# Optimization experiments

Measured on AMD Instinct MI355X. Metric: run time of the kernel, lower is better.

The kernel has to match this reference:

```python
import jax, jax.numpy as jnp
import numpy as np

D_MODEL = 1024
D_STATE = 64
D_CONV = 4
EXPAND = 2
HEADDIM = 64
FFN_MULT = 3
MEM_DIM = 256
D_INNER = EXPAND * D_MODEL            # 2048
NHEADS = D_INNER // HEADDIM           # 32
CONV_DIM = D_INNER + 2 * D_STATE      # x, B, C channels through the causal conv
D_IN_PROJ = 2 * D_INNER + 2 * D_STATE + NHEADS  # z, xBC, dt
FFN_HID = FFN_MULT * D_MODEL


def _rms(x, eps=1e-6):
    return x * jax.lax.rsqrt(jnp.mean(x * x, axis=-1, keepdims=True) + eps)


def _mamba2(u, in_proj_w, conv_w, conv_b, dt_bias, A_log, D_param, mnorm_w, out_proj_w):
    # u: [B, L, d_model]
    Bsz, L, _ = u.shape
    zxbcdt = u @ in_proj_w.T                                  # [B, L, D_IN_PROJ]
    z = zxbcdt[..., :D_INNER]                                 # gate branch
    xBC = zxbcdt[..., D_INNER:D_INNER + CONV_DIM]
    dt = zxbcdt[..., D_INNER + CONV_DIM:]                     # [B, L, H]
    # causal depthwise conv1d (kernel D_CONV) + silu
    xp = jnp.pad(xBC, ((0, 0), (D_CONV - 1, 0), (0, 0)))
    xBC = sum(xp[:, k:k + L, :] * conv_w[:, k] for k in range(D_CONV)) + conv_b
    xBC = jax.nn.silu(xBC)
    xh = xBC[..., :D_INNER].reshape(Bsz, L, NHEADS, HEADDIM)  # [B, L, H, P]
    Bm = xBC[..., D_INNER:D_INNER + D_STATE]                  # [B, L, N] (ngroups=1)
    Cm = xBC[..., D_INNER + D_STATE:]                         # [B, L, N]
    dt = jax.nn.softplus(dt + dt_bias)                        # [B, L, H]
    dA = jnp.exp(dt * (-jnp.exp(A_log)))                      # [B, L, H]

    def step(h, inp):
        # h: [B, H, P, N]
        da, dtt, xt, bt, ct = inp
        h = da[:, :, None, None] * h + jnp.einsum('bh,bhp,bn->bhpn', dtt, xt, bt)
        y = jnp.einsum('bhpn,bn->bhp', h, ct)
        return h, y

    h0 = jnp.zeros((Bsz, NHEADS, HEADDIM, D_STATE), u.dtype)
    xs = (jnp.moveaxis(dA, 1, 0), jnp.moveaxis(dt, 1, 0), jnp.moveaxis(xh, 1, 0),
          jnp.moveaxis(Bm, 1, 0), jnp.moveaxis(Cm, 1, 0))
    _, ys = jax.lax.scan(step, h0, xs)                        # ys: [L, B, H, P]
    y = jnp.moveaxis(ys, 0, 1) + D_param[None, None, :, None] * xh
    y = y.reshape(Bsz, L, D_INNER)
    y = _rms(y * jax.nn.silu(z)) * mnorm_w                    # RMSNormGated
    return y @ out_proj_w.T


def setup_inputs() -> dict:
    key = jax.random.key(0)
    ks = jax.random.split(key, 12)
    B, L = 1, 2048
    s = 0.02
    return {
        'x': jax.random.normal(ks[0], (B, L, D_MODEL), jnp.float32),
        'x0': jax.random.normal(ks[1], (B, L, D_MODEL), jnp.float32),
        'mem': jax.random.normal(ks[2], (B, MEM_DIM), jnp.float32),
        'resid_mix': jnp.stack([jnp.ones(D_MODEL), jnp.zeros(D_MODEL)]),
        'ssm_scale': jnp.ones(D_MODEL),
        'mlp_scale': jnp.ones(D_MODEL),
        'ssm_norm_w': jnp.ones(D_MODEL),
        'ffn_norm_w': jnp.ones(D_MODEL),
        'in_proj_w': jax.random.normal(ks[3], (D_IN_PROJ, D_MODEL), jnp.float32) * s,
        'conv_w': jax.random.normal(ks[4], (CONV_DIM, D_CONV), jnp.float32) * 0.2,
        'conv_b': jnp.zeros(CONV_DIM),
        'dt_bias': jax.random.uniform(ks[5], (NHEADS,), jnp.float32, -2.0, 0.0),
        'A_log': jnp.log(jnp.linspace(1.0, 16.0, NHEADS).astype(jnp.float32)),
        'D_param': jnp.ones(NHEADS),
        'mnorm_w': jnp.ones(D_INNER),
        'out_proj_w': jax.random.normal(ks[6], (D_MODEL, D_INNER), jnp.float32) * s,
        'gate_up_w': jax.random.normal(ks[7], (2 * FFN_HID, D_MODEL), jnp.float32) * s,
        'down_w': jax.random.normal(ks[8], (D_MODEL, FFN_HID), jnp.float32) * s,
    }


def reference(x, x0, mem, resid_mix, ssm_scale, mlp_scale, ssm_norm_w, ffn_norm_w,
              in_proj_w, conv_w, conv_b, dt_bias, A_log, D_param, mnorm_w,
              out_proj_w, gate_up_w, down_w):
    # residual mixing (USE_MEMORY=0, so mem path is inert)
    x = resid_mix[0][None, None, :] * x + resid_mix[1][None, None, :] * x0
    y = _mamba2(_rms(x) * ssm_norm_w, in_proj_w, conv_w, conv_b, dt_bias,
                A_log, D_param, mnorm_w, out_proj_w)
    x = x + ssm_scale[None, None, :] * y
    # SwiGLU FFN
    h = _rms(x) * ffn_norm_w
    gu = h @ gate_up_w.T
    gate, up = jnp.split(gu, 2, axis=-1)
    x = x + mlp_scale[None, None, :] * ((jax.nn.silu(gate) * up) @ down_w.T)
    return x
```

## Files before the change

### kernel.cpp

```cpp
#include <hip/hip_runtime.h>
#include <hip/hip_bf16.h>
#include <math.h>

#define LSEQ 2048
#define DMODEL 1024
#define DINNER 2048
#define NHEADS 32
#define HEADDIM 64
#define DSTATE 64
#define CONVDIM 2176
#define XBCDT_W 2304
#define FFNHID 3072

typedef float f32x4 __attribute__((ext_vector_type(4)));
typedef __bf16 bf16x8 __attribute__((ext_vector_type(8)));
typedef __hip_bfloat16 bf16;

__device__ __forceinline__ float siluf(float x){ return x / (1.0f + expf(-x)); }

#define GLOAD_LDS16(gp, lp) __builtin_amdgcn_global_load_lds( \
    (const __attribute__((address_space(1))) void*)(gp), \
    (__attribute__((address_space(3))) void*)(lp), 16, 0, 0)

__device__ __forceinline__ float block_reduce_sum_256(float v){
  #pragma unroll
  for (int o = 32; o > 0; o >>= 1) v += __shfl_down(v, o, 64);
  __shared__ float sh[4];
  int lane = threadIdx.x & 63;
  int w = threadIdx.x >> 6;
  if (lane == 0) sh[w] = v;
  __syncthreads();
  return sh[0] + sh[1] + sh[2] + sh[3];
}

__device__ __forceinline__ ushort bf16bits(float f){
  __hip_bfloat16 h = __float2bfloat16(f);
  return *reinterpret_cast<ushort*>(&h);
}
__device__ __forceinline__ float bfu(ushort u){
  union { float f; unsigned int i; } w; w.i = ((unsigned int)u) << 16; return w.f;
}

__device__ __forceinline__ int swz64(int r, int c){
  return r*64 + ((((c>>3) ^ (r&7)))<<3) + (c&7);
}

__global__ __launch_bounds__(256) void k_castmix(
    const float* __restrict__ w0, const float* __restrict__ w1,
    const float* __restrict__ w2, const float* __restrict__ w3,
    bf16* __restrict__ d0, bf16* __restrict__ d1,
    bf16* __restrict__ d2, bf16* __restrict__ d3,
    const float* __restrict__ x, const float* __restrict__ x0,
    const float* __restrict__ rm, const float* __restrict__ nw,
    float* __restrict__ xres, bf16* __restrict__ u)
{
  int tid = threadIdx.x;
  if (blockIdx.x < 15616){
    int idx = blockIdx.x * 256 + tid;
    const float* s; bf16* d; int valid;
    if (idx < 1114112)      { s = w0; d = d0; valid = 1089536; }
    else if (idx < 1638400) { idx -= 1114112; s = w1; d = d1; valid = 524288; }
    else if (idx < 3211264) { idx -= 1638400; s = w2; d = d2; valid = 1572864; }
    else                    { idx -= 3211264; s = w3; d = d3; valid = 786432; }
    float4 v = (idx < valid) ? *(const float4*)(s + (size_t)idx * 4)
                             : make_float4(0.f, 0.f, 0.f, 0.f);
    ushort4 r;
    r.x = bf16bits(v.x); r.y = bf16bits(v.y); r.z = bf16bits(v.z); r.w = bf16bits(v.w);
    *(ushort4*)(d + (size_t)idx * 4) = r;
    return;
  }
  int row = blockIdx.x - 15616;
  float4 xv  = ((const float4*)(x  + (size_t)row * DMODEL))[tid];
  float4 x0v = ((const float4*)(x0 + (size_t)row * DMODEL))[tid];
  float4 r0 = ((const float4*)rm)[tid];
  float4 r1 = ((const float4*)(rm + DMODEL))[tid];
  float4 a;
  a.x = r0.x*xv.x + r1.x*x0v.x; a.y = r0.y*xv.y + r1.y*x0v.y;
  a.z = r0.z*xv.z + r1.z*x0v.z; a.w = r0.w*xv.w + r1.w*x0v.w;
  ((float4*)(xres + (size_t)row * DMODEL))[tid] = a;
  float ss = a.x*a.x + a.y*a.y + a.z*a.z + a.w*a.w;
  ss = block_reduce_sum_256(ss);
  float inv = rsqrtf(ss / (float)DMODEL + 1e-6f);
  float4 nv = ((const float4*)nw)[tid];
  ushort4 o;
  o.x = bf16bits(a.x*inv*nv.x); o.y = bf16bits(a.y*inv*nv.y);
  o.z = bf16bits(a.z*inv*nv.z); o.w = bf16bits(a.w*inv*nv.w);
  *(ushort4*)(u + (size_t)row * DMODEL + tid*4) = o;
}

__device__ __forceinline__ void xcdswz2(int &bx, int &by){
  int gx = gridDim.x;
  int nblk = gx * gridDim.y;
  int flat = by * gx + bx;
  flat = (flat & 7) * (nblk >> 3) + (flat >> 3);
  by = flat / gx; bx = flat - by * gx;
}

__device__ __forceinline__ void gemm_mainloop128(
    const bf16* __restrict__ A, const bf16* __restrict__ W,
    int ld, int Klen, bf16* As, bf16* Ws, f32x4 acc[4][4])
{
  int tid = threadIdx.x, lane = tid & 63, wid = tid >> 6;
  int wm = (wid >> 1) * 64, wn = (wid & 1) * 64;
  int r16 = lane & 15, g8 = lane >> 4;
  int srow = lane >> 2;
  int scol = ((lane & 3) ^ (srow & 3) ^ ((srow >> 2) & 3)) * 8;
  const bf16* ga0 = A + (size_t)(wid*32 + srow) * ld + scol;
  const bf16* ga1 = ga0 + (size_t)16 * ld;
  const bf16* gw0 = W + (size_t)(wid*32 + srow) * ld + scol;
  const bf16* gw1 = gw0 + (size_t)16 * ld;
  GLOAD_LDS16(ga0, As + wid*1024);
  GLOAD_LDS16(ga1, As + wid*1024 + 512);
  GLOAD_LDS16(gw0, Ws + wid*1024);
  GLOAD_LDS16(gw1, Ws + wid*1024 + 512);
  __syncthreads();
  int cur = 0;
  int s4 = ((r16 & 3) ^ ((r16 >> 2) & 3)) * 8;
  for (int k0 = 0; k0 < Klen; k0 += 32){
    if (k0 + 32 < Klen){
      int nb = (cur ^ 1) * 4096;
      GLOAD_LDS16(ga0 + k0 + 32, As + nb + wid*1024);
      GLOAD_LDS16(ga1 + k0 + 32, As + nb + wid*1024 + 512);
      GLOAD_LDS16(gw0 + k0 + 32, Ws + nb + wid*1024);
      GLOAD_LDS16(gw1 + k0 + 32, Ws + nb + wid*1024 + 512);
    }
    int cb = cur * 4096;
    bf16x8 af[4], bfr[4];
    #pragma unroll
    for (int i = 0; i < 4; ++i)
      af[i] = *(const bf16x8*)(As + cb + (wm + i*16 + r16)*32 + (g8*8 ^ s4));
    #pragma unroll
    for (int j = 0; j < 4; ++j)
      bfr[j] = *(const bf16x8*)(Ws + cb + (wn + j*16 + r16)*32 + (g8*8 ^ s4));
    #pragma unroll
    for (int i = 0; i < 4; ++i)
      #pragma unroll
      for (int j = 0; j < 4; ++j)
        acc[i][j] = __builtin_amdgcn_mfma_f32_16x16x32_bf16(af[i], bfr[j], acc[i][j], 0, 0, 0);
    __syncthreads();
    cur ^= 1;
  }
}

__global__ __launch_bounds__(256) void k_gemm_inproj(
    const bf16* __restrict__ A, const bf16* __restrict__ Wfull,
    bf16* __restrict__ zbuf, bf16* __restrict__ xbcdt)
{
  __shared__ __align__(16) bf16 As[2*4096];
  __shared__ __align__(16) bf16 Ws[2*4096];
  int bx = blockIdx.x, by = blockIdx.y;
  xcdswz2(bx, by);
  f32x4 acc[4][4];
  #pragma unroll
  for (int i = 0; i < 4; ++i)
    #pragma unroll
    for (int j = 0; j < 4; ++j) acc[i][j] = (f32x4){0.f,0.f,0.f,0.f};
  gemm_mainloop128(A + (size_t)(by*128)*DMODEL, Wfull + (size_t)(bx*128)*DMODEL,
                   DMODEL, DMODEL, As, Ws, acc);
  int tid = threadIdx.x, lane = tid & 63, wid = tid >> 6;
  int wm = (wid >> 1) * 64, wn = (wid & 1) * 64;
  int r16 = lane & 15, g8 = lane >> 4;
  bf16* Cp; int ldc, col0;
  if (bx < 16){ Cp = zbuf;  ldc = DINNER;  col0 = bx*128; }
  else        { Cp = xbcdt; ldc = XBCDT_W; col0 = (bx-16)*128; }
  #pragma unroll
  for (int i = 0; i < 4; ++i){
    int row = by*128 + wm + i*16 + g8*4;
    #pragma unroll
    for (int j = 0; j < 4; ++j){
      int col = col0 + wn + j*16 + r16;
      #pragma unroll
      for (int r = 0; r < 4; ++r)
        Cp[(size_t)(row + r) * ldc + col] = __float2bfloat16(acc[i][j][r]);
    }
  }
}

__global__ __launch_bounds__(256) void k_gemm_splitk(
    const bf16* __restrict__ A, const bf16* __restrict__ W,
    float* __restrict__ P, int Kfull, int Kq, int N)
{
  __shared__ __align__(16) bf16 As[2*4096];
  __shared__ __align__(16) bf16 Ws[2*4096];
  int gx = gridDim.x, gxy = gx * gridDim.y;
  int nblk = gxy * gridDim.z;
  int flat = blockIdx.z * gxy + blockIdx.y * gx + blockIdx.x;
  flat = (flat & 7) * (nblk >> 3) + (flat >> 3);
  int z = flat / gxy; int rem = flat - z * gxy;
  int by = rem / gx, bx = rem - by * gx;
  f32x4 acc[4][4];
  #pragma unroll
  for (int i = 0; i < 4; ++i)
    #pragma unroll
    for (int j = 0; j < 4; ++j) acc[i][j] = (f32x4){0.f,0.f,0.f,0.f};
  gemm_mainloop128(A + (size_t)(by*128)*Kfull + z*Kq,
                   W + (size_t)(bx*128)*Kfull + z*Kq,
                   Kfull, Kq, As, Ws, acc);
  float* Pz = P + (size_t)z * LSEQ * N;
  int tid = threadIdx.x, lane = tid & 63, wid = tid >> 6;
  int wm = (wid >> 1) * 64, wn = (wid & 1) * 64;
  int r16 = lane & 15, g8 = lane >> 4;
  #pragma unroll
  for (int i = 0; i < 4; ++i){
    int row = by*128 + wm + i*16 + g8*4;
    #pragma unroll
    for (int j = 0; j < 4; ++j){
      int col = bx*128 + wn + j*16 + r16;
      #pragma unroll
      for (int r = 0; r < 4; ++r)
        Pz[(size_t)(row + r) * N + col] = acc[i][j][r];
    }
  }
}

__global__ __launch_bounds__(256) void k_gemm_ffn(
    const bf16* __restrict__ A, const bf16* __restrict__ Wg, const bf16* __restrict__ Wu,
    bf16* __restrict__ act, int K)
{
  __shared__ __align__(16) bf16 As[2*4096];
  __shared__ __align__(16) bf16 Ws[2*4096];
  int bx = blockIdx.x, by = blockIdx.y;
  xcdswz2(bx, by);
  int tid = threadIdx.x, lane = tid & 63, wid = tid >> 6;
  int wm = (wid >> 1) * 64, wc = (wid & 1) * 32;
  int r16 = lane & 15, g8 = lane >> 4;
  int srow = lane >> 2;
  int scol = ((lane & 3) ^ (srow & 3) ^ ((srow >> 2) & 3)) * 8;
  const bf16* ga0 = A + (size_t)(by*128 + wid*32 + srow) * K + scol;
  const bf16* ga1 = ga0 + (size_t)16 * K;
  const bf16* gwsrc = (wid < 2) ? Wg : Wu;
  const bf16* gw0 = gwsrc + (size_t)(bx*64 + (wid & 1)*32 + srow) * K + scol;
  const bf16* gw1 = gw0 + (size_t)16 * K;
  f32x4 accg[4][2], accu[4][2];
  #pragma unroll
  for (int i = 0; i < 4; ++i)
    #pragma unroll
    for (int j = 0; j < 2; ++j){
      accg[i][j] = (f32x4){0.f,0.f,0.f,0.f};
      accu[i][j] = (f32x4){0.f,0.f,0.f,0.f};
    }
  GLOAD_LDS16(ga0, As + wid*1024);
  GLOAD_LDS16(ga1, As + wid*1024 + 512);
  GLOAD_LDS16(gw0, Ws + wid*1024);
  GLOAD_LDS16(gw1, Ws + wid*1024 + 512);
  __syncthreads();
  int cur = 0;
  int s4 = ((r16 & 3) ^ ((r16 >> 2) & 3)) * 8;
  for (int k0 = 0; k0 < K; k0 += 32){
    if (k0 + 32 < K){
      int nb = (cur ^ 1) * 4096;
      GLOAD_LDS16(ga0 + k0 + 32, As + nb + wid*1024);
      GLOAD_LDS16(ga1 + k0 + 32, As + nb + wid*1024 + 512);
      GLOAD_LDS16(gw0 + k0 + 32, Ws + nb + wid*1024);
      GLOAD_LDS16(gw1 + k0 + 32, Ws + nb + wid*1024 + 512);
    }
    int cb = cur * 4096;
    bf16x8 af[4], gf[2], uf[2];
    #pragma unroll
    for (int i = 0; i < 4; ++i)
      af[i] = *(const bf16x8*)(As + cb + (wm + i*16 + r16)*32 + (g8*8 ^ s4));
    #pragma unroll
    for (int j = 0; j < 2; ++j){
      int gr = wc + j*16 + r16;
      int ur = 64 + wc + j*16 + r16;
      gf[j] = *(const bf16x8*)(Ws + cb + gr*32 + (g8*8 ^ s4));
      uf[j] = *(const bf16x8*)(Ws + cb + ur*32 + (g8*8 ^ s4));
    }
    #pragma unroll
    for (int i = 0; i < 4; ++i)
      #pragma unroll
      for (int j = 0; j < 2; ++j){
        accg[i][j] = __builtin_amdgcn_mfma_f32_16x16x32_bf16(af[i], gf[j], accg[i][j], 0, 0, 0);
        accu[i][j] = __builtin_amdgcn_mfma_f32_16x16x32_bf16(af[i], uf[j], accu[i][j], 0, 0, 0);
      }
    __syncthreads();
    cur ^= 1;
  }
  #pragma unroll
  for (int i = 0; i < 4; ++i){
    int row = by*128 + wm + i*16 + g8*4;
    #pragma unroll
    for (int j = 0; j < 2; ++j){
      int col = bx*64 + wc + j*16 + r16;
      #pragma unroll
      for (int r = 0; r < 4; ++r){
        float g = accg[i][j][r], u = accu[i][j][r];
        act[(size_t)(row + r) * FFNHID + col] = __float2bfloat16(siluf(g) * u);
      }
    }
  }
}

__global__ __launch_bounds__(256) void k_convdt(
    const bf16* __restrict__ xbcdt, const float* __restrict__ cw,
    const float* __restrict__ cb, const float* __restrict__ dtb,
    const float* __restrict__ alog, bf16* __restrict__ xbc,
    float* __restrict__ dtv, float* __restrict__ lav)
{
  int idx = blockIdx.x * 256 + threadIdx.x;
  int l = idx / 552, q = idx - l * 552;
  if (l >= LSEQ) return;
  if (q < 544){
    int c = q * 4;
    float4 bv = *(const float4*)(cb + c);
    float acc0 = bv.x, acc1 = bv.y, acc2 = bv.z, acc3 = bv.w;
    float4 w0 = *(const float4*)(cw + (size_t)(c+0)*4);
    float4 w1 = *(const float4*)(cw + (size_t)(c+1)*4);
    float4 w2 = *(const float4*)(cw + (size_t)(c+2)*4);
    float4 w3 = *(const float4*)(cw + (size_t)(c+3)*4);
    const float* w0p = (const float*)&w0;
    const float* w1p = (const float*)&w1;
    const float* w2p = (const float*)&w2;
    const float* w3p = (const float*)&w3;
    #pragma unroll
    for (int k = 0; k < 4; ++k){
      int t = l + k - 3;
      if (t < 0) continue;
      ushort4 rv = *(const ushort4*)(xbcdt + (size_t)t * XBCDT_W + c);
      acc0 = fmaf(bfu(rv.x), w0p[k], acc0);
      acc1 = fmaf(bfu(rv.y), w1p[k], acc1);
      acc2 = fmaf(bfu(rv.z), w2p[k], acc2);
      acc3 = fmaf(bfu(rv.w), w3p[k], acc3);
    }
    ushort4 o;
    o.x = bf16bits(siluf(acc0)); o.y = bf16bits(siluf(acc1));
    o.z = bf16bits(siluf(acc2)); o.w = bf16bits(siluf(acc3));
    *(ushort4*)(xbc + (size_t)l * CONVDIM + c) = o;
  } else {
    int h0 = (q - 544) * 4;
    ushort4 rv = *(const ushort4*)(xbcdt + (size_t)l * XBCDT_W + CONVDIM + h0);
    float raws[4] = { bfu(rv.x), bfu(rv.y), bfu(rv.z), bfu(rv.w) };
    #pragma unroll
    for (int i = 0; i < 4; ++i){
      float raw = raws[i] + dtb[h0 + i];
      float d = (raw > 20.f) ? raw : log1pf(expf(raw));
      dtv[l * NHEADS + h0 + i] = d;
      lav[l * NHEADS + h0 + i] = -expf(alog[h0 + i]) * d;
    }
  }
}

__global__ __launch_bounds__(256) void k_scanA(
    const bf16* __restrict__ xbc, const float* __restrict__ dtv,
    const float* __restrict__ lav, float* __restrict__ T, float* __restrict__ ctot)
{
  __shared__ __bf16 sXw[4096];
  __shared__ __bf16 sBt[4096];
  __shared__ float scum[64], swt[64];
  int h = blockIdx.x >> 5, c = blockIdx.x & 31;
  int tid = threadIdx.x, t0 = c * 64;
  if (tid < 64){
    float cum = lav[(size_t)(t0 + tid) * NHEADS + h];
    #pragma unroll
    for (int o = 1; o < 64; o <<= 1){
      float v = __shfl_up(cum, o, 64);
      if (tid >= o) cum += v;
    }
    scum[tid] = cum;
  }
  __syncthreads();
  float Lc = scum[63];
  if (tid < 64)
    swt[tid] = expf(Lc - scum[tid]) * dtv[(size_t)(t0 + tid) * NHEADS + h];
  __syncthreads();
  for (int idx = tid; idx < 512; idx += 256){
    int j = idx >> 3, n0 = (idx & 7) * 8;
    const bf16* rb = xbc + (size_t)(t0 + j) * CONVDIM;
    bf16x8 x8 = *(const bf16x8*)(rb + h * HEADDIM + n0);
    bf16x8 b8 = *(const bf16x8*)(rb + DINNER + n0);
    float wj = swt[j];
    #pragma unroll
    for (int e = 0; e < 8; ++e){
      sXw[swz64(n0 + e, j)] = (__bf16)((float)x8[e] * wj);
      sBt[swz64(n0 + e, j)] = b8[e];
    }
  }
  __syncthreads();
  int lane = tid & 63, wid = tid >> 6;
  int wr = (wid >> 1) * 32, wc = (wid & 1) * 32;
  int r16 = lane & 15, g8 = lane >> 4;
  f32x4 acc[2][2];
  #pragma unroll
  for (int i = 0; i < 2; ++i)
    #pragma unroll
    for (int j = 0; j < 2; ++j) acc[i][j] = (f32x4){0.f,0.f,0.f,0.f};
  #pragma unroll
  for (int kk = 0; kk < 2; ++kk){
    int ks = kk*4 + g8;
    bf16x8 a[2], b[2];
    #pragma unroll
    for (int i = 0; i < 2; ++i){
      int row = wr + i*16 + r16;
      a[i] = *(const bf16x8*)(sXw + row*64 + ((ks ^ (row&7))<<3));
    }
    #pragma unroll
    for (int j = 0; j < 2; ++j){
      int row = wc + j*16 + r16;
      b[j] = *(const bf16x8*)(sBt + row*64 + ((ks ^ (row&7))<<3));
    }
    #pragma unroll
    for (int i = 0; i < 2; ++i)
      #pragma unroll
      for (int j = 0; j < 2; ++j)
        acc[i][j] = __builtin_amdgcn_mfma_f32_16x16x32_bf16(a[i], b[j], acc[i][j], 0, 0, 0);
  }
  float* Tb = T + (size_t)blockIdx.x * 4096;
  #pragma unroll
  for (int i = 0; i < 2; ++i)
    #pragma unroll
    for (int j = 0; j < 2; ++j)
      #pragma unroll
      for (int r = 0; r < 4; ++r){
        int p = wr + i*16 + g8*4 + r, n = wc + j*16 + r16;
        Tb[p*64 + n] = acc[i][j][r];
      }
  if (tid == 0) ctot[blockIdx.x] = expf(Lc);
}

__global__ __launch_bounds__(256) void k_scanB(float* __restrict__ T, const float* __restrict__ ctot)
{
  int h = blockIdx.x >> 3, e = blockIdx.x & 7;
  int tid = threadIdx.x;
  size_t off = (size_t)e * 512 + tid * 2;
  float s0 = 0.f, s1 = 0.f;
  for (int c0 = 0; c0 < 32; c0 += 8){
    float2 tv[8]; float cts[8];
    #pragma unroll
    for (int q = 0; q < 8; ++q){
      cts[q] = ctot[h * 32 + c0 + q];
      tv[q] = *(const float2*)&T[(size_t)(h * 32 + c0 + q) * 4096 + off];
    }
    #pragma unroll
    for (int q = 0; q < 8; ++q){
      size_t base = (size_t)(h * 32 + c0 + q) * 4096 + off;
      *(float2*)&T[base] = make_float2(s0, s1);
      s0 = fmaf(cts[q], s0, tv[q].x);
      s1 = fmaf(cts[q], s1, tv[q].y);
    }
  }
}

__global__ __launch_bounds__(256) void k_scanC(
    const bf16* __restrict__ xbc, const float* __restrict__ Sin,
    const float* __restrict__ dtv, const float* __restrict__ lav,
    const float* __restrict__ Dp, bf16* __restrict__ y)
{
  __shared__ __bf16 sC[4096];
  __shared__ __bf16 sBS[4096];
  __shared__ __bf16 sXt[4096];
  __shared__ __bf16 sXr[4096];
  __shared__ __bf16 sSb[4096];
  __shared__ float scum[64], sdt[64];
  int h = blockIdx.x >> 5, c = blockIdx.x & 31;
  int tid = threadIdx.x, t0 = c * 64;
  if (tid < 64){
    float cum = lav[(size_t)(t0 + tid) * NHEADS + h];
    #pragma unroll
    for (int o = 1; o < 64; o <<= 1){
      float v = __shfl_up(cum, o, 64);
      if (tid >= o) cum += v;
    }
    scum[tid] = cum;
    sdt[tid] = dtv[(size_t)(t0 + tid) * NHEADS + h];
  }
  for (int idx = tid; idx < 512; idx += 256){
    int j = idx >> 3, n0 = (idx & 7) * 8;
    const bf16* rb = xbc + (size_t)(t0 + j) * CONVDIM;
    bf16x8 x8 = *(const bf16x8*)(rb + h * HEADDIM + n0);
    bf16x8 c8 = *(const bf16x8*)(rb + DINNER + DSTATE + n0);
    bf16x8 b8 = *(const bf16x8*)(rb + DINNER + n0);
    *(bf16x8*)(sC  + swz64(j, n0)) = c8;
    *(bf16x8*)(sBS + swz64(j, n0)) = b8;
    *(bf16x8*)(sXr + swz64(j, n0)) = x8;
    const float* sp = Sin + (size_t)blockIdx.x * 4096 + j*64 + n0;
    float4 s0 = *(const float4*)sp;
    float4 s1 = *(const float4*)(sp + 4);
    bf16x8 sv;
    sv[0] = (__bf16)s0.x; sv[1] = (__bf16)s0.y; sv[2] = (__bf16)s0.z; sv[3] = (__bf16)s0.w;
    sv[4] = (__bf16)s1.x; sv[5] = (__bf16)s1.y; sv[6] = (__bf16)s1.z; sv[7] = (__bf16)s1.w;
    *(bf16x8*)(sSb + swz64(j, n0)) = sv;
    #pragma unroll
    for (int e = 0; e < 8; ++e)
      sXt[swz64(n0 + e, j)] = x8[e];
  }
  __syncthreads();
  int lane = tid & 63, wid = tid >> 6;
  int wr = (wid >> 1) * 32, wc = (wid & 1) * 32;
  int r16 = lane & 15, g8 = lane >> 4;
  f32x4 gacc[2][2];
  #pragma unroll
  for (int i = 0; i < 2; ++i)
    #pragma unroll
    for (int j = 0; j < 2; ++j) gacc[i][j] = (f32x4){0.f,0.f,0.f,0.f};
  #pragma unroll
  for (int kk = 0; kk < 2; ++kk){
    int ks = kk*4 + g8;
    bf16x8 a[2], b[2];
    #pragma unroll
    for (int i = 0; i < 2; ++i){
      int row = wr + i*16 + r16;
      a[i] = *(const bf16x8*)(sC + row*64 + ((ks ^ (row&7))<<3));
    }
    #pragma unroll
    for (int j = 0; j < 2; ++j){
      int row = wc + j*16 + r16;
      b[j] = *(const bf16x8*)(sBS + row*64 + ((ks ^ (row&7))<<3));
    }
    #pragma unroll
    for (int i = 0; i < 2; ++i)
      #pragma unroll
      for (int j = 0; j < 2; ++j)
        gacc[i][j] = __builtin_amdgcn_mfma_f32_16x16x32_bf16(a[i], b[j], gacc[i][j], 0, 0, 0);
  }
  __syncthreads();
  #pragma unroll
  for (int i = 0; i < 2; ++i)
    #pragma unroll
    for (int j = 0; j < 2; ++j)
      #pragma unroll
      for (int r = 0; r < 4; ++r){
        int i_ = wr + i*16 + g8*4 + r, j_ = wc + j*16 + r16;
        float v = (j_ <= i_) ? gacc[i][j][r] * expf(scum[i_] - scum[j_]) * sdt[j_] : 0.f;
        sBS[swz64(i_, j_)] = (__bf16)v;
      }
  __syncthreads();
  f32x4 a1[2][2], a2[2][2];
  #pragma unroll
  for (int i = 0; i < 2; ++i)
    #pragma unroll
    for (int j = 0; j < 2; ++j){
      a1[i][j] = (f32x4){0.f,0.f,0.f,0.f};
      a2[i][j] = (f32x4){0.f,0.f,0.f,0.f};
    }
  #pragma unroll
  for (int kk = 0; kk < 2; ++kk){
    int ks = kk*4 + g8;
    bf16x8 sa[2], xa[2], ca[2], sb[2];
    #pragma unroll
    for (int i = 0; i < 2; ++i){
      int row = wr + i*16 + r16;
      sa[i] = *(const bf16x8*)(sBS + row*64 + ((ks ^ (row&7))<<3));
      ca[i] = *(const bf16x8*)(sC  + row*64 + ((ks ^ (row&7))<<3));
    }
    #pragma unroll
    for (int j = 0; j < 2; ++j){
      int row = wc + j*16 + r16;
      xa[j] = *(const bf16x8*)(sXt + row*64 + ((ks ^ (row&7))<<3));
      sb[j] = *(const bf16x8*)(sSb + row*64 + ((ks ^ (row&7))<<3));
    }
    #pragma unroll
    for (int i = 0; i < 2; ++i)
      #pragma unroll
      for (int j = 0; j < 2; ++j){
        a1[i][j] = __builtin_amdgcn_mfma_f32_16x16x32_bf16(sa[i], xa[j], a1[i][j], 0, 0, 0);
        a2[i][j] = __builtin_amdgcn_mfma_f32_16x16x32_bf16(ca[i], sb[j], a2[i][j], 0, 0, 0);
      }
  }
  float Dh = Dp[h];
  #pragma unroll
  for (int i = 0; i < 2; ++i)
    #pragma unroll
    for (int r = 0; r < 4; ++r){
      int i_ = wr + i*16 + g8*4 + r;
      float wi = expf(scum[i_]);
      #pragma unroll
      for (int j = 0; j < 2; ++j){
        int p_ = wc + j*16 + r16;
        float xv = (float)sXr[swz64(i_, p_)];
        y[(size_t)(t0 + i_) * DINNER + h * HEADDIM + p_] =
            __float2bfloat16(a1[i][j][r] + wi * a2[i][j][r] + Dh * xv);
      }
    }
}

__global__ __launch_bounds__(256) void k_gate_rms(
    const bf16* __restrict__ y, const bf16* __restrict__ zbuf,
    const float* __restrict__ mw, bf16* __restrict__ yn)
{
  int row = blockIdx.x, tid = threadIdx.x;
  bf16x8 yv = *(const bf16x8*)(y    + (size_t)row * DINNER + tid*8);
  bf16x8 zv = *(const bf16x8*)(zbuf + (size_t)row * DINNER + tid*8);
  float g[8]; float ss = 0.f;
  #pragma unroll
  for (int e = 0; e < 8; ++e){
    float gv = (float)yv[e] * siluf((float)zv[e]);
    g[e] = gv; ss += gv * gv;
  }
  ss = block_reduce_sum_256(ss);
  float inv = rsqrtf(ss / (float)DINNER + 1e-6f);
  float4 m0 = ((const float4*)mw)[tid*2];
  float4 m1 = ((const float4*)mw)[tid*2 + 1];
  const float* mp = (const float*)&m0;
  bf16x8 o;
  #pragma unroll
  for (int e = 0; e < 4; ++e) o[e] = (__bf16)(g[e] * inv * mp[e]);
  mp = (const float*)&m1;
  #pragma unroll
  for (int e = 0; e < 4; ++e) o[4+e] = (__bf16)(g[4+e] * inv * mp[e]);
  *(bf16x8*)(yn + (size_t)row * DINNER + tid*8) = o;
}

__global__ __launch_bounds__(256) void k_res_rms(
    const float* __restrict__ xres, const float* __restrict__ yoP,
    const float* __restrict__ scale, const float* __restrict__ nw,
    float* __restrict__ x2, bf16* __restrict__ hb)
{
  int row = blockIdx.x, tid = threadIdx.x;
  const size_t PS = (size_t)LSEQ * DMODEL;
  float4 xv = ((const float4*)(xres + (size_t)row * DMODEL))[tid];
  float4 y0 = ((const float4*)(yoP          + (size_t)row * DMODEL))[tid];
  float4 y1 = ((const float4*)(yoP +   PS   + (size_t)row * DMODEL))[tid];
  float4 y2 = ((const float4*)(yoP + 2*PS   + (size_t)row * DMODEL))[tid];
  float4 y3 = ((const float4*)(yoP + 3*PS   + (size_t)row * DMODEL))[tid];
  float4 sv = ((const float4*)scale)[tid];
  float4 a;
  a.x = xv.x + sv.x*(y0.x+y1.x+y2.x+y3.x);
  a.y = xv.y + sv.y*(y0.y+y1.y+y2.y+y3.y);
  a.z = xv.z + sv.z*(y0.z+y1.z+y2.z+y3.z);
  a.w = xv.w + sv.w*(y0.w+y1.w+y2.w+y3.w);
  ((float4*)(x2 + (size_t)row * DMODEL))[tid] = a;
  float ss = a.x*a.x + a.y*a.y + a.z*a.z + a.w*a.w;
  ss = block_reduce_sum_256(ss);
  float inv = rsqrtf(ss / (float)DMODEL + 1e-6f);
  float4 nv = ((const float4*)nw)[tid];
  ushort4 o;
  o.x = bf16bits(a.x*inv*nv.x); o.y = bf16bits(a.y*inv*nv.y);
  o.z = bf16bits(a.z*inv*nv.z); o.w = bf16bits(a.w*inv*nv.w);
  *(ushort4*)(hb + (size_t)row * DMODEL + tid*4) = o;
}

__global__ __launch_bounds__(256) void k_final(
    const float* __restrict__ x2, const float* __restrict__ dP,
    const float* __restrict__ mscale, float* __restrict__ out)
{
  int i4 = blockIdx.x * 256 + threadIdx.x;
  const size_t PS4 = (size_t)LSEQ * DMODEL / 4;
  float4 xv = ((const float4*)x2)[i4];
  float4 a  = ((const float4*)dP)[i4];
  float4 b  = ((const float4*)dP)[i4 + PS4];
  float4 c  = ((const float4*)dP)[i4 + 2*PS4];
  float4 d  = ((const float4*)dP)[i4 + 3*PS4];
  float4 mv = ((const float4*)mscale)[i4 & 255];
  float4 o;
  o.x = xv.x + mv.x*(a.x+b.x+c.x+d.x);
  o.y = xv.y + mv.y*(a.y+b.y+c.y+d.y);
  o.z = xv.z + mv.z*(a.z+b.z+c.z+d.z);
  o.w = xv.w + mv.w*(a.w+b.w+c.w+d.w);
  ((float4*)out)[i4] = o;
}

extern "C" void kernel_launch(void* const* d_in, const int* in_sizes, int n_in,
                              void* d_out, int out_size, void* d_ws, size_t ws_size,
                              hipStream_t stream)
{
  const float* x      = (const float*)d_in[0];
  const float* x0     = (const float*)d_in[1];
  const float* rm     = (const float*)d_in[3];
  const float* sscale = (const float*)d_in[4];
  const float* mscale = (const float*)d_in[5];
  const float* snw    = (const float*)d_in[6];
  const float* fnw    = (const float*)d_in[7];
  const float* win    = (const float*)d_in[8];
  const float* cw     = (const float*)d_in[9];
  const float* cb     = (const float*)d_in[10];
  const float* dtb    = (const float*)d_in[11];
  const float* alog   = (const float*)d_in[12];
  const float* Dp     = (const float*)d_in[13];
  const float* mnw    = (const float*)d_in[14];
  const float* wout   = (const float*)d_in[15];
  const float* wgu    = (const float*)d_in[16];
  const float* wdn    = (const float*)d_in[17];
  float* out = (float*)d_out;

  const size_t MB = 1024ull * 1024ull;
  char* ws = (char*)d_ws;
  bf16*  woutb = (bf16*) (ws + 0*MB);
  bf16*  wgub  = (bf16*) (ws + 4*MB);
  bf16*  wdnb  = (bf16*) (ws + 16*MB);
  float* xres  = (float*)(ws + 22*MB);
  bf16*  winb  = (bf16*) (ws + 30*MB);
  bf16*  u     = (bf16*) (ws + 39*MB);
  float* dtv   = (float*)(ws + 39*MB);
  float* lav   = (float*)(ws + 39*MB + 256*1024);
  bf16*  hb    = (bf16*) (ws + 39*MB);
  bf16*  zbuf  = (bf16*) (ws + 43*MB);
  float* x2    = (float*)(ws + 43*MB);
  bf16*  xbcdt = (bf16*) (ws + 59*MB);
  bf16*  yb    = (bf16*) (ws + 59*MB);
  float* yoP   = (float*)(ws + 59*MB);
  bf16*  act   = (bf16*) (ws + 59*MB);
  float* dP    = (float*)(ws + 71*MB);
  bf16*  xbc   = (bf16*) (ws + 77*MB);
  float* T     = (float*)(ws + 95*MB);
  bf16*  yn    = (bf16*) (ws + 95*MB);
  float* ctot  = (float*)(ws + 112*MB);

  dim3 blk(256);
  k_castmix<<<17664, blk, 0, stream>>>(win, wout, wgu, wdn, winb, woutb, wgub, wdnb,
                                       x, x0, rm, snw, xres, u);
  k_gemm_inproj<<<dim3(34,16), blk, 0, stream>>>(u, winb, zbuf, xbcdt);
  k_convdt<<<(LSEQ*552)/256, blk, 0, stream>>>(xbcdt, cw, cb, dtb, alog, xbc, dtv, lav);
  k_scanA<<<NHEADS*32, blk, 0, stream>>>(xbc, dtv, lav, T, ctot);
  k_scanB<<<NHEADS*8, blk, 0, stream>>>(T, ctot);
  k_scanC<<<NHEADS*32, blk, 0, stream>>>(xbc, T, dtv, lav, Dp, yb);
  k_gate_rms<<<LSEQ, blk, 0, stream>>>(yb, zbuf, mnw, yn);
  k_gemm_splitk<<<dim3(8,16,4), blk, 0, stream>>>(yn, woutb, yoP, DINNER, DINNER/4, DMODEL);
  k_res_rms<<<LSEQ, blk, 0, stream>>>(xres, yoP, sscale, fnw, x2, hb);
  k_gemm_ffn<<<dim3(48,16), blk, 0, stream>>>(hb, wgub, wgub + (size_t)FFNHID*DMODEL, act, DMODEL);
  k_gemm_splitk<<<dim3(8,16,4), blk, 0, stream>>>(act, wdnb, dP, FFNHID, FFNHID/4, DMODEL);
  k_final<<<2048, blk, 0, stream>>>(x2, dP, mscale, out);
}
```

Baseline: 196.0 us.

## Replace split-K partial buffers with atomic accumulation and store scan states in bf16

The two split-K GEMMs now atomically add their partial results into a single fp32 output instead of writing four partial planes. The down-projection atomically adds scaled results straight into the final output, which k_res_rms has already filled with the residual, so k_final and the x2 buffer go away. The inter-chunk scan state T is stored in bf16 rather than fp32, which halves its traffic and removes a conversion in scanC. The cost is atomic contention, nondeterministic summation order, an extra memset, and lower precision in the scan carry.

```diff
diff --git a/kernel.cpp b/kernel.cpp
--- a/kernel.cpp
+++ b/kernel.cpp
@@ -176,9 +176,9 @@
   }
 }
 
-__global__ __launch_bounds__(256) void k_gemm_splitk(
+__global__ __launch_bounds__(256) void k_gemm_out(
     const bf16* __restrict__ A, const bf16* __restrict__ W,
-    float* __restrict__ P, int Kfull, int Kq, int N)
+    float* __restrict__ Y, int Kfull, int Kq, int N)
 {
   __shared__ __align__(16) bf16 As[2*4096];
   __shared__ __align__(16) bf16 Ws[2*4096];
@@ -196,7 +196,6 @@
   gemm_mainloop128(A + (size_t)(by*128)*Kfull + z*Kq,
                    W + (size_t)(bx*128)*Kfull + z*Kq,
                    Kfull, Kq, As, Ws, acc);
-  float* Pz = P + (size_t)z * LSEQ * N;
   int tid = threadIdx.x, lane = tid & 63, wid = tid >> 6;
   int wm = (wid >> 1) * 64, wn = (wid & 1) * 64;
   int r16 = lane & 15, g8 = lane >> 4;
@@ -208,7 +207,45 @@
       int col = bx*128 + wn + j*16 + r16;
       #pragma unroll
       for (int r = 0; r < 4; ++r)
-        Pz[(size_t)(row + r) * N + col] = acc[i][j][r];
+        atomicAdd(&Y[(size_t)(row + r) * N + col], acc[i][j][r]);
+    }
+  }
+}
+
+__global__ __launch_bounds__(256) void k_gemm_down(
+    const bf16* __restrict__ A, const bf16* __restrict__ W,
+    const float* __restrict__ mscale, float* __restrict__ out,
+    int Kfull, int Kq)
+{
+  __shared__ __align__(16) bf16 As[2*4096];
+  __shared__ __align__(16) bf16 Ws[2*4096];
+  int gx = gridDim.x, gxy = gx * gridDim.y;
+  int nblk = gxy * gridDim.z;
+  int flat = blockIdx.z * gxy + blockIdx.y * gx + blockIdx.x;
+  flat = (flat & 7) * (nblk >> 3) + (flat >> 3);
+  int z = flat / gxy; int rem = flat - z * gxy;
+  int by = rem / gx, bx = rem - by * gx;
+  f32x4 acc[4][4];
+  #pragma unroll
+  for (int i = 0; i < 4; ++i)
+    #pragma unroll
+    for (int j = 0; j < 4; ++j) acc[i][j] = (f32x4){0.f,0.f,0.f,0.f};
+  gemm_mainloop128(A + (size_t)(by*128)*Kfull + z*Kq,
+                   W + (size_t)(bx*128)*Kfull + z*Kq,
+                   Kfull, Kq, As, Ws, acc);
+  int tid = threadIdx.x, lane = tid & 63, wid = tid >> 6;
+  int wm = (wid >> 1) * 64, wn = (wid & 1) * 64;
+  int r16 = lane & 15, g8 = lane >> 4;
+  #pragma unroll
+  for (int i = 0; i < 4; ++i){
+    int row = by*128 + wm + i*16 + g8*4;
+    #pragma unroll
+    for (int j = 0; j < 4; ++j){
+      int col = bx*128 + wn + j*16 + r16;
+      float mv = mscale[col];
+      #pragma unroll
+      for (int r = 0; r < 4; ++r)
+        atomicAdd(&out[(size_t)(row + r) * DMODEL + col], mv * acc[i][j][r]);
     }
   }
 }
@@ -342,7 +379,7 @@
 
 __global__ __launch_bounds__(256) void k_scanA(
     const bf16* __restrict__ xbc, const float* __restrict__ dtv,
-    const float* __restrict__ lav, float* __restrict__ T, float* __restrict__ ctot)
+    const float* __restrict__ lav, bf16* __restrict__ T, float* __restrict__ ctot)
 {
   __shared__ __bf16 sXw[4096];
   __shared__ __bf16 sBt[4096];
@@ -404,7 +441,7 @@
       for (int j = 0; j < 2; ++j)
         acc[i][j] = __builtin_amdgcn_mfma_f32_16x16x32_bf16(a[i], b[j], acc[i][j], 0, 0, 0);
   }
-  float* Tb = T + (size_t)blockIdx.x * 4096;
+  bf16* Tb = T + (size_t)blockIdx.x * 4096;
   #pragma unroll
   for (int i = 0; i < 2; ++i)
     #pragma unroll
@@ -412,36 +449,37 @@
       #pragma unroll
       for (int r = 0; r < 4; ++r){
         int p = wr + i*16 + g8*4 + r, n = wc + j*16 + r16;
-        Tb[p*64 + n] = acc[i][j][r];
+        Tb[p*64 + n] = __float2bfloat16(acc[i][j][r]);
       }
   if (tid == 0) ctot[blockIdx.x] = expf(Lc);
 }
 
-__global__ __launch_bounds__(256) void k_scanB(float* __restrict__ T, const float* __restrict__ ctot)
+__global__ __launch_bounds__(256) void k_scanB(bf16* __restrict__ T, const float* __restrict__ ctot)
 {
   int h = blockIdx.x >> 3, e = blockIdx.x & 7;
   int tid = threadIdx.x;
   size_t off = (size_t)e * 512 + tid * 2;
   float s0 = 0.f, s1 = 0.f;
   for (int c0 = 0; c0 < 32; c0 += 8){
-    float2 tv[8]; float cts[8];
+    ushort2 tv[8]; float cts[8];
     #pragma unroll
     for (int q = 0; q < 8; ++q){
       cts[q] = ctot[h * 32 + c0 + q];
-      tv[q] = *(const float2*)&T[(size_t)(h * 32 + c0 + q) * 4096 + off];
+      tv[q] = *(const ushort2*)&T[(size_t)(h * 32 + c0 + q) * 4096 + off];
     }
     #pragma unroll
     for (int q = 0; q < 8; ++q){
       size_t base = (size_t)(h * 32 + c0 + q) * 4096 + off;
-      *(float2*)&T[base] = make_float2(s0, s1);
-      s0 = fmaf(cts[q], s0, tv[q].x);
-      s1 = fmaf(cts[q], s1, tv[q].y);
+      ushort2 sv; sv.x = bf16bits(s0); sv.y = bf16bits(s1);
+      *(ushort2*)&T[base] = sv;
+      s0 = fmaf(cts[q], s0, bfu(tv[q].x));
+      s1 = fmaf(cts[q], s1, bfu(tv[q].y));
     }
   }
 }
 
 __global__ __launch_bounds__(256) void k_scanC(
-    const bf16* __restrict__ xbc, const float* __restrict__ Sin,
+    const bf16* __restrict__ xbc, const bf16* __restrict__ Sin,
     const float* __restrict__ dtv, const float* __restrict__ lav,
     const float* __restrict__ Dp, bf16* __restrict__ y)
 {
@@ -463,6 +501,7 @@
     scum[tid] = cum;
     sdt[tid] = dtv[(size_t)(t0 + tid) * NHEADS + h];
   }
+  const bf16* Tb = Sin + (size_t)blockIdx.x * 4096;
   for (int idx = tid; idx < 512; idx += 256){
     int j = idx >> 3, n0 = (idx & 7) * 8;
     const bf16* rb = xbc + (size_t)(t0 + j) * CONVDIM;
@@ -472,13 +511,7 @@
     *(bf16x8*)(sC  + swz64(j, n0)) = c8;
     *(bf16x8*)(sBS + swz64(j, n0)) = b8;
     *(bf16x8*)(sXr + swz64(j, n0)) = x8;
-    const float* sp = Sin + (size_t)blockIdx.x * 4096 + j*64 + n0;
-    float4 s0 = *(const float4*)sp;
-    float4 s1 = *(const float4*)(sp + 4);
-    bf16x8 sv;
-    sv[0] = (__bf16)s0.x; sv[1] = (__bf16)s0.y; sv[2] = (__bf16)s0.z; sv[3] = (__bf16)s0.w;
-    sv[4] = (__bf16)s1.x; sv[5] = (__bf16)s1.y; sv[6] = (__bf16)s1.z; sv[7] = (__bf16)s1.w;
-    *(bf16x8*)(sSb + swz64(j, n0)) = sv;
+    *(bf16x8*)(sSb + swz64(j, n0)) = *(const bf16x8*)(Tb + j*64 + n0);
     #pragma unroll
     for (int e = 0; e < 8; ++e)
       sXt[swz64(n0 + e, j)] = x8[e];
@@ -601,24 +634,18 @@
 }
 
 __global__ __launch_bounds__(256) void k_res_rms(
-    const float* __restrict__ xres, const float* __restrict__ yoP,
+    const float* __restrict__ xres, const float* __restrict__ yo,
     const float* __restrict__ scale, const float* __restrict__ nw,
-    float* __restrict__ x2, bf16* __restrict__ hb)
+    float* __restrict__ out, bf16* __restrict__ hb)
 {
   int row = blockIdx.x, tid = threadIdx.x;
-  const size_t PS = (size_t)LSEQ * DMODEL;
   float4 xv = ((const float4*)(xres + (size_t)row * DMODEL))[tid];
-  float4 y0 = ((const float4*)(yoP          + (size_t)row * DMODEL))[tid];
-  float4 y1 = ((const float4*)(yoP +   PS   + (size_t)row * DMODEL))[tid];
-  float4 y2 = ((const float4*)(yoP + 2*PS   + (size_t)row * DMODEL))[tid];
-  float4 y3 = ((const float4*)(yoP + 3*PS   + (size_t)row * DMODEL))[tid];
+  float4 yv = ((const float4*)(yo   + (size_t)row * DMODEL))[tid];
   float4 sv = ((const float4*)scale)[tid];
   float4 a;
-  a.x = xv.x + sv.x*(y0.x+y1.x+y2.x+y3.x);
-  a.y = xv.y + sv.y*(y0.y+y1.y+y2.y+y3.y);
-  a.z = xv.z + sv.z*(y0.z+y1.z+y2.z+y3.z);
-  a.w = xv.w + sv.w*(y0.w+y1.w+y2.w+y3.w);
-  ((float4*)(x2 + (size_t)row * DMODEL))[tid] = a;
+  a.x = xv.x + sv.x*yv.x; a.y = xv.y + sv.y*yv.y;
+  a.z = xv.z + sv.z*yv.z; a.w = xv.w + sv.w*yv.w;
+  ((float4*)(out + (size_t)row * DMODEL))[tid] = a;
   float ss = a.x*a.x + a.y*a.y + a.z*a.z + a.w*a.w;
   ss = block_reduce_sum_256(ss);
   float inv = rsqrtf(ss / (float)DMODEL + 1e-6f);
@@ -627,26 +654,6 @@
   o.x = bf16bits(a.x*inv*nv.x); o.y = bf16bits(a.y*inv*nv.y);
   o.z = bf16bits(a.z*inv*nv.z); o.w = bf16bits(a.w*inv*nv.w);
   *(ushort4*)(hb + (size_t)row * DMODEL + tid*4) = o;
-}
-
-__global__ __launch_bounds__(256) void k_final(
-    const float* __restrict__ x2, const float* __restrict__ dP,
-    const float* __restrict__ mscale, float* __restrict__ out)
-{
-  int i4 = blockIdx.x * 256 + threadIdx.x;
-  const size_t PS4 = (size_t)LSEQ * DMODEL / 4;
-  float4 xv = ((const float4*)x2)[i4];
-  float4 a  = ((const float4*)dP)[i4];
-  float4 b  = ((const float4*)dP)[i4 + PS4];
-  float4 c  = ((const float4*)dP)[i4 + 2*PS4];
-  float4 d  = ((const float4*)dP)[i4 + 3*PS4];
-  float4 mv = ((const float4*)mscale)[i4 & 255];
-  float4 o;
-  o.x = xv.x + mv.x*(a.x+b.x+c.x+d.x);
-  o.y = xv.y + mv.y*(a.y+b.y+c.y+d.y);
-  o.z = xv.z + mv.z*(a.z+b.z+c.z+d.z);
-  o.w = xv.w + mv.w*(a.w+b.w+c.w+d.w);
-  ((float4*)out)[i4] = o;
 }
 
 extern "C" void kernel_launch(void* const* d_in, const int* in_sizes, int n_in,
@@ -684,14 +691,12 @@
   float* lav   = (float*)(ws + 39*MB + 256*1024);
   bf16*  hb    = (bf16*) (ws + 39*MB);
   bf16*  zbuf  = (bf16*) (ws + 43*MB);
-  float* x2    = (float*)(ws + 43*MB);
   bf16*  xbcdt = (bf16*) (ws + 59*MB);
   bf16*  yb    = (bf16*) (ws + 59*MB);
-  float* yoP   = (float*)(ws + 59*MB);
+  float* yo    = (float*)(ws + 59*MB);
   bf16*  act   = (bf16*) (ws + 59*MB);
-  float* dP    = (float*)(ws + 71*MB);
   bf16*  xbc   = (bf16*) (ws + 77*MB);
-  float* T     = (float*)(ws + 95*MB);
+  bf16*  T     = (bf16*) (ws + 95*MB);
   bf16*  yn    = (bf16*) (ws + 95*MB);
   float* ctot  = (float*)(ws + 112*MB);
 
@@ -704,9 +709,9 @@
   k_scanB<<<NHEADS*8, blk, 0, stream>>>(T, ctot);
   k_scanC<<<NHEADS*32, blk, 0, stream>>>(xbc, T, dtv, lav, Dp, yb);
   k_gate_rms<<<LSEQ, blk, 0, stream>>>(yb, zbuf, mnw, yn);
-  k_gemm_splitk<<<dim3(8,16,4), blk, 0, stream>>>(yn, woutb, yoP, DINNER, DINNER/4, DMODEL);
-  k_res_rms<<<LSEQ, blk, 0, stream>>>(xres, yoP, sscale, fnw, x2, hb);
+  hipMemsetAsync(yo, 0, (size_t)LSEQ * DMODEL * sizeof(float), stream);
+  k_gemm_out<<<dim3(8,16,4), blk, 0, stream>>>(yn, woutb, yo, DINNER, DINNER/4, DMODEL);
+  k_res_rms<<<LSEQ, blk, 0, stream>>>(xres, yo, sscale, fnw, out, hb);
   k_gemm_ffn<<<dim3(48,16), blk, 0, stream>>>(hb, wgub, wgub + (size_t)FFNHID*DMODEL, act, DMODEL);
-  k_gemm_splitk<<<dim3(8,16,4), blk, 0, stream>>>(act, wdnb, dP, FFNHID, FFNHID/4, DMODEL);
-  k_final<<<2048, blk, 0, stream>>>(x2, dP, mscale, out);
-}
+  k_gemm_down<<<dim3(8,16,4), blk, 0, stream>>>(act, wdnb, mscale, out, FFNHID, FFNHID/4);
+}
```

Result: slower. 226.3 us (+15.5%).
